# Kernel optimization log

Measured on AMD Instinct MI355X. Metric: run time of the kernel, lower is better.

The kernel has to match this reference:

```python
import jax, jax.numpy as jnp
import numpy as np

B, S, H = 32, 512, 768
N, E, P = 4096, 131072, 65536
HEADS1, C1 = 4, 128
HEADS2, C2 = 1, 64
NUM_REL, REL_HID = 6, 256
NER_HID, NER_LAB = 256, 9
LRELU_SLOPE = 0.2  # PyG GATConv default negative_slope
LN_EPS = 1e-5


def setup_inputs() -> dict:
    key = jax.random.key(0)
    ks = jax.random.split(key, 24)
    sc = 0.02
    inp = {
        'sequence_output': jax.random.normal(ks[0], (B, S, H), jnp.float32),
        'ent_start': jax.random.randint(ks[1], (N,), 0, S - 8),
        'ent_len': jax.random.randint(ks[2], (N,), 0, 8),
        'ent_batch': jax.random.randint(ks[3], (N,), 0, B),
        'edge_index': jax.random.randint(ks[4], (2, E), 0, N),
        'pair_idx': jax.random.randint(ks[5], (P, 2), 0, N),
        'W1': jax.random.normal(ks[6], (H, HEADS1 * C1), jnp.float32) * sc,
        'a_src1': jax.random.normal(ks[7], (HEADS1, C1), jnp.float32) * sc,
        'a_dst1': jax.random.normal(ks[8], (HEADS1, C1), jnp.float32) * sc,
        'b1': jnp.zeros((HEADS1 * C1,), jnp.float32),
        'W2': jax.random.normal(ks[9], (HEADS1 * C1, HEADS2 * C2), jnp.float32) * sc,
        'a_src2': jax.random.normal(ks[10], (HEADS2, C2), jnp.float32) * sc,
        'a_dst2': jax.random.normal(ks[11], (HEADS2, C2), jnp.float32) * sc,
        'b2': jnp.zeros((HEADS2 * C2,), jnp.float32),
        # 6 per-relation classifiers: Linear(128,256)+LN+ReLU+Linear(256,1)
        'relW1': jax.random.normal(ks[12], (NUM_REL, 2 * C2, REL_HID), jnp.float32) * sc,
        'relb1': jnp.zeros((NUM_REL, REL_HID), jnp.float32),
        'ln_g': jnp.ones((NUM_REL, REL_HID), jnp.float32),
        'ln_b': jnp.zeros((NUM_REL, REL_HID), jnp.float32),
        'relW2': jax.random.normal(ks[13], (NUM_REL, REL_HID, 1), jnp.float32) * sc,
        'relb2': jnp.zeros((NUM_REL, 1), jnp.float32),
        # NER head: Linear(768,256)+ReLU+Linear(256,9)
        'nerW1': jax.random.normal(ks[14], (H, NER_HID), jnp.float32) * sc,
        'nerb1': jnp.zeros((NER_HID,), jnp.float32),
        'nerW2': jax.random.normal(ks[15], (NER_HID, NER_LAB), jnp.float32) * sc,
        'nerb2': jnp.zeros((NER_LAB,), jnp.float32),
    }
    return inp


def _gat(x, src, dst, W, a_src, a_dst, b, heads, ch, n):
    # PyG GATConv: per-head linear, additive attention, softmax over incoming edges
    h = (x @ W).reshape(n, heads, ch)                      # [N,Hd,C]
    e_src = jnp.sum(h * a_src, axis=-1)                    # [N,Hd]
    e_dst = jnp.sum(h * a_dst, axis=-1)
    e = jax.nn.leaky_relu(e_src[src] + e_dst[dst], LRELU_SLOPE)  # [E,Hd]
    m = jax.ops.segment_max(e, dst, num_segments=n)
    ex = jnp.exp(e - m[dst])
    denom = jax.ops.segment_sum(ex, dst, num_segments=n)
    alpha = ex / denom[dst]                                # [E,Hd]
    out = jax.ops.segment_sum(alpha[:, :, None] * h[src], dst, num_segments=n)
    return out.reshape(n, heads * ch) + b


def reference(sequence_output, ent_start, ent_len, ent_batch, edge_index, pair_idx,
              W1, a_src1, a_dst1, b1, W2, a_src2, a_dst2, b2,
              relW1, relb1, ln_g, ln_b, relW2, relb2,
              nerW1, nerb1, nerW2, nerb2):
    n = ent_start.shape[0]
    # NER head on the full sequence
    ner_logits = jax.nn.relu(sequence_output @ nerW1 + nerb1) @ nerW2 + nerb2  # [B,S,9]
    # Entity-span mean pooling via exclusive prefix sums (inclusive span start..start+len)
    csum = jnp.cumsum(sequence_output, axis=1)
    csum = jnp.concatenate([jnp.zeros((B, 1, H), sequence_output.dtype), csum], axis=1)  # [B,S+1,H]
    ent_end = ent_start + ent_len
    span_sum = csum[ent_batch, ent_end + 1] - csum[ent_batch, ent_start]  # [N,H]
    x = span_sum / (ent_len + 1).astype(span_sum.dtype)[:, None]
    # add self loops (PyG GATConv default add_self_loops=True)
    loops = jnp.arange(n, dtype=edge_index.dtype)
    src = jnp.concatenate([edge_index[0], loops])
    dst = jnp.concatenate([edge_index[1], loops])
    x = _gat(x, src, dst, W1, a_src1, a_dst1, b1, HEADS1, C1, n)
    x = jax.nn.relu(x)  # dropout p=0.3 is identity in eval mode
    x = _gat(x, src, dst, W2, a_src2, a_dst2, b2, HEADS2, C2, n)  # [N,64]
    # Pair features: cat(x[e1], x[e2]) -> [P,128]
    pair_feat = jnp.concatenate([x[pair_idx[:, 0]], x[pair_idx[:, 1]]], axis=-1)
    # All 6 relation classifiers, vectorized over the relation dim
    hid = jnp.einsum('pf,rfk->rpk', pair_feat, relW1) + relb1[:, None, :]  # [6,P,256]
    mu = jnp.mean(hid, axis=-1, keepdims=True)
    var = jnp.mean(jnp.square(hid - mu), axis=-1, keepdims=True)
    hid = (hid - mu) * jax.lax.rsqrt(var + LN_EPS) * ln_g[:, None, :] + ln_b[:, None, :]
    hid = jax.nn.relu(hid)
    rel_logits = (jnp.einsum('rpk,rko->rpo', hid, relW2) + relb2[:, None, :])[..., 0]  # [6,P]
    return ner_logits, rel_logits
```

## Files before the change

### kernel.cpp

```cpp
#include <hip/hip_runtime.h>
#include <math.h>

#define LRELU 0.2f

constexpr int Bn = 32, Sn = 512, Hn = 768, Nn = 4096, En = 131072, Pn = 65536;
constexpr int ET = En + Nn;

typedef __attribute__((ext_vector_type(8))) short bf16x8;
typedef __attribute__((ext_vector_type(4))) float f32x4;

constexpr size_t OFF_X0  = 0;
constexpr size_t OFF_UV  = 0;
constexpr size_t OFF_H1  = 4194304;
constexpr size_t OFF_X1  = OFF_H1  + 2097152;
constexpr size_t OFF_H2  = OFF_X1  + 2097152;
constexpr size_t OFF_X2  = OFF_H2  + 262144;
constexpr size_t OFF_ES1 = OFF_X2  + 262144;
constexpr size_t OFF_ED1 = OFF_ES1 + 16384;
constexpr size_t OFF_ES2 = OFF_ED1 + 16384;
constexpr size_t OFF_ED2 = OFF_ES2 + 4096;
constexpr size_t OFF_ROW = OFF_ED2 + 4096;
constexpr size_t OFF_CUR = OFF_ROW + 4104;
constexpr size_t OFF_EDG = OFF_CUR + 4096;
constexpr size_t OFF_W1S = OFF_EDG + 135168;
constexpr size_t OFF_NW1S = OFF_W1S + 196608;
constexpr size_t OFF_W2S = OFF_NW1S + 98304;

__device__ __forceinline__ short f2bf(float f) {
  union { float f; unsigned u; } x; x.f = f;
  unsigned r = x.u + 0x7fff + ((x.u >> 16) & 1);
  return (short)(r >> 16);
}
__device__ __forceinline__ float bf2f(short s) {
  union { unsigned u; float f; } x;
  x.u = ((unsigned)(unsigned short)s) << 16;
  return x.f;
}

__global__ __launch_bounds__(256) void span_pool_k(
    const float* __restrict__ seq, const int* __restrict__ est,
    const int* __restrict__ eln, const int* __restrict__ ebt,
    float* __restrict__ x0) {
  int idx = blockIdx.x * 256 + threadIdx.x;
  if (idx >= Nn * (Hn / 4)) return;
  int e = idx / (Hn / 4);
  int c = (idx % (Hn / 4)) * 4;
  int s0 = est[e], L = eln[e] + 1, b = ebt[e];
  const float* p = seq + ((size_t)b * Sn + s0) * Hn + c;
  float ax = 0, ay = 0, az = 0, aw = 0;
  for (int i = 0; i < L; ++i) {
    float4 v = *(const float4*)(p + (size_t)i * Hn);
    ax += v.x; ay += v.y; az += v.z; aw += v.w;
  }
  float inv = 1.0f / (float)L;
  float4 o; o.x = ax * inv; o.y = ay * inv; o.z = az * inv; o.w = aw * inv;
  *(float4*)&x0[(size_t)e * Hn + c] = o;
}

template <int EPI, int NTW, int KC>
__global__ __launch_bounds__(256) void mfma_gemm_k(
    const float* __restrict__ A, const short* __restrict__ Bswz,
    float* __restrict__ C, const float* __restrict__ bias,
    int M, int K, int N) {
  constexpr int RS = KC + 8;
  __shared__ short at[64 * RS];
  int t = threadIdx.x;
  size_t rowb = (size_t)blockIdx.x * 64;
  int colb = blockIdx.y * (64 * NTW);
  int w = t >> 6, lane = t & 63, quad = lane >> 4, id = lane & 15;
  f32x4 acc[4][NTW];
#pragma unroll
  for (int mt = 0; mt < 4; ++mt)
#pragma unroll
    for (int nt = 0; nt < NTW; ++nt) acc[mt][nt] = (f32x4){0.f, 0.f, 0.f, 0.f};

  for (int k0 = 0; k0 < K; k0 += KC) {
    constexpr int CH = 64 * KC / 8 / 256;
#pragma unroll
    for (int i = 0; i < CH; ++i) {
      int cid = t + i * 256;
      int p = cid / (KC / 8), o8 = (cid % (KC / 8)) * 8;
      const float* src = &A[(rowb + p) * (size_t)K + k0 + o8];
      float4 v0 = *(const float4*)src;
      float4 v1 = *(const float4*)(src + 4);
      bf16x8 bv;
      bv[0] = f2bf(v0.x); bv[1] = f2bf(v0.y); bv[2] = f2bf(v0.z); bv[3] = f2bf(v0.w);
      bv[4] = f2bf(v1.x); bv[5] = f2bf(v1.y); bv[6] = f2bf(v1.z); bv[7] = f2bf(v1.w);
      *(bf16x8*)&at[p * RS + o8] = bv;
    }
    __syncthreads();
#pragma unroll
    for (int kk = 0; kk < KC / 32; ++kk) {
      bf16x8 af[4], bfr[NTW];
#pragma unroll
      for (int mt = 0; mt < 4; ++mt)
        af[mt] = *(const bf16x8*)&at[(mt * 16 + id) * RS + kk * 32 + quad * 8];
#pragma unroll
      for (int nt = 0; nt < NTW; ++nt) {
        int ntg = (colb >> 4) + w * NTW + nt;
        bfr[nt] = *(const bf16x8*)&Bswz[(((size_t)(k0 >> 5) + kk) * (N >> 4) + ntg) * 512 + lane * 8];
      }
#pragma unroll
      for (int mt = 0; mt < 4; ++mt)
#pragma unroll
        for (int nt = 0; nt < NTW; ++nt)
          acc[mt][nt] = __builtin_amdgcn_mfma_f32_16x16x32_bf16(af[mt], bfr[nt], acc[mt][nt], 0, 0, 0);
    }
    __syncthreads();
  }
#pragma unroll
  for (int nt = 0; nt < NTW; ++nt) {
    int col = colb + w * (16 * NTW) + nt * 16 + id;
#pragma unroll
    for (int mt = 0; mt < 4; ++mt) {
#pragma unroll
      for (int reg = 0; reg < 4; ++reg) {
        size_t row = rowb + mt * 16 + quad * 4 + reg;
        float v = acc[mt][nt][reg];
        if (EPI == 3) {
          int r = col >> 9, rem = col & 511;
          if (rem < 256) v += bias[(r << 8) + rem];
          ((short*)C)[((size_t)r * Nn + row) * 512 + rem] = f2bf(v);
        } else if (EPI == 2) {
          ((short*)C)[row * (size_t)N + col] = f2bf(v);
        } else {
          C[row * (size_t)N + col] = v;
        }
      }
    }
  }
}

template <int MT>
__global__ __launch_bounds__(256) void ner_fused_k(
    const float* __restrict__ A, const short* __restrict__ Bswz,
    const float* __restrict__ W2, const float* __restrict__ b1,
    const float* __restrict__ b2, float* __restrict__ out) {
  constexpr int K = 768;
  constexpr int RS = 136, HS = 264, WS = 260;
  constexpr int MW = MT / 16;
  __shared__ short at[MT * RS];
  __shared__ short hid[MT * HS];
  __shared__ float w2t[9 * WS];
  __shared__ float b2l[9];
  int t = threadIdx.x;
  size_t rowb = (size_t)blockIdx.x * MT;
  for (int u = t; u < 2304; u += 256) {
    int k = u / 9, jj = u % 9;
    w2t[jj * WS + k] = W2[u];
  }
  if (t < 9) b2l[t] = b2[t];
  int w = t >> 6, lane = t & 63, quad = lane >> 4, id = lane & 15;
  f32x4 acc[MW][4];
#pragma unroll
  for (int mt = 0; mt < MW; ++mt)
#pragma unroll
    for (int nt = 0; nt < 4; ++nt) acc[mt][nt] = (f32x4){0.f, 0.f, 0.f, 0.f};

  for (int k0 = 0; k0 < K; k0 += 128) {
#pragma unroll
    for (int i = 0; i < MT / 16; ++i) {
      int cid = t + i * 256;
      int p = cid >> 4, o8 = (cid & 15) * 8;
      const float* src = &A[(rowb + p) * (size_t)K + k0 + o8];
      float4 v0 = *(const float4*)src;
      float4 v1 = *(const float4*)(src + 4);
      bf16x8 bv;
      bv[0] = f2bf(v0.x); bv[1] = f2bf(v0.y); bv[2] = f2bf(v0.z); bv[3] = f2bf(v0.w);
      bv[4] = f2bf(v1.x); bv[5] = f2bf(v1.y); bv[6] = f2bf(v1.z); bv[7] = f2bf(v1.w);
      *(bf16x8*)&at[p * RS + o8] = bv;
    }
    __syncthreads();
#pragma unroll
    for (int kk = 0; kk < 4; ++kk) {
      bf16x8 af[MW], bfr[4];
#pragma unroll
      for (int mt = 0; mt < MW; ++mt)
        af[mt] = *(const bf16x8*)&at[(mt * 16 + id) * RS + kk * 32 + quad * 8];
#pragma unroll
      for (int nt = 0; nt < 4; ++nt) {
        int ntg = w * 4 + nt;
        bfr[nt] = *(const bf16x8*)&Bswz[(((size_t)(k0 >> 5) + kk) * 16 + ntg) * 512 + lane * 8];
      }
#pragma unroll
      for (int mt = 0; mt < MW; ++mt)
#pragma unroll
        for (int nt = 0; nt < 4; ++nt)
          acc[mt][nt] = __builtin_amdgcn_mfma_f32_16x16x32_bf16(af[mt], bfr[nt], acc[mt][nt], 0, 0, 0);
    }
    __syncthreads();
  }
#pragma unroll
  for (int nt = 0; nt < 4; ++nt) {
    int col = w * 64 + nt * 16 + id;
    float bb = b1[col];
#pragma unroll
    for (int mt = 0; mt < MW; ++mt)
#pragma unroll
      for (int reg = 0; reg < 4; ++reg) {
        int row = mt * 16 + quad * 4 + reg;
        hid[row * HS + col] = f2bf(fmaxf(acc[mt][nt][reg] + bb, 0.f));
      }
  }
  __syncthreads();
  for (int u = t; u < MT * 9; u += 256) {
    int row = u / 9, jj = u % 9;
    const short* hp = &hid[row * HS];
    const float* wp = &w2t[jj * WS];
    float a = 0.f;
#pragma unroll
    for (int k8 = 0; k8 < 256; k8 += 8) {
      bf16x8 hv = *(const bf16x8*)&hp[k8];
      float4 w0 = *(const float4*)&wp[k8];
      float4 w1 = *(const float4*)&wp[k8 + 4];
      a += bf2f(hv[0]) * w0.x + bf2f(hv[1]) * w0.y + bf2f(hv[2]) * w0.z + bf2f(hv[3]) * w0.w;
      a += bf2f(hv[4]) * w1.x + bf2f(hv[5]) * w1.y + bf2f(hv[6]) * w1.z + bf2f(hv[7]) * w1.w;
    }
    out[(rowb + row) * 9 + jj] = a + b2l[jj];
  }
}

__device__ __forceinline__ void swz_store(short* __restrict__ o, int k, int n, int N, float v) {
  int kk = k >> 5, quad = (k >> 3) & 3, j = k & 7, ntg = n >> 4, id = n & 15;
  o[(((size_t)kk * (N >> 4)) + ntg) * 512 + (quad * 16 + id) * 8 + j] = f2bf(v);
}

__global__ void swz_all_k(const float* __restrict__ W1, const float* __restrict__ nW1,
                          const float* __restrict__ W2, short* __restrict__ w1s,
                          short* __restrict__ nw1s, short* __restrict__ w2s) {
  int i = blockIdx.x * 256 + threadIdx.x;
  if (i < 768 * 512) {
    swz_store(w1s, i / 512, i % 512, 512, W1[i]);
  } else if (i < 768 * 512 + 768 * 256) {
    int i2 = i - 768 * 512;
    swz_store(nw1s, i2 / 256, i2 % 256, 256, nW1[i2]);
  } else if (i < 768 * 512 + 768 * 256 + 512 * 64) {
    int i2 = i - (768 * 512 + 768 * 256);
    swz_store(w2s, i2 / 64, i2 % 64, 64, W2[i2]);
  }
}

__global__ void swz_uv_k(const float* __restrict__ rW1, short* __restrict__ o) {
  int i = blockIdx.x * 256 + threadIdx.x;
  if (i >= 6 * 128 * 256) return;
  int n = i & 255, k = (i >> 8) & 127, r = i >> 15;
  int c = r * 512 + (k >> 6) * 256 + n;
  int kr = k & 63;
  int kk = kr >> 5, quad = (kr >> 3) & 3, j = kr & 7, ntg = c >> 4, id = c & 15;
  o[(((size_t)kk * 192) + ntg) * 512 + (quad * 16 + id) * 8 + j] = f2bf(rW1[i]);
}

template <int HD, int C>
__global__ __launch_bounds__(256) void coef_b_k(
    const short* __restrict__ h, const float* __restrict__ a_src,
    const float* __restrict__ a_dst, float* __restrict__ es, float* __restrict__ ed) {
  int idx = blockIdx.x * 256 + threadIdx.x;
  if (idx >= Nn * HD) return;
  int n = idx / HD, hd = idx % HD;
  const short* hp = h + (size_t)n * HD * C + hd * C;
  const float* sp = a_src + hd * C;
  const float* dp = a_dst + hd * C;
  float s = 0, d = 0;
  for (int c = 0; c < C; c += 8) {
    bf16x8 v = *(const bf16x8*)(hp + c);
#pragma unroll
    for (int k = 0; k < 8; ++k) {
      float f = bf2f(v[k]);
      s += f * sp[c + k];
      d += f * dp[c + k];
    }
  }
  es[idx] = s; ed[idx] = d;
}

__global__ void zero_k(int* __restrict__ p, int n) {
  int i = blockIdx.x * 256 + threadIdx.x;
  if (i < n) p[i] = 0;
}

__global__ void count_k(const int* __restrict__ eidx, int* __restrict__ cnt) {
  int i = blockIdx.x * 256 + threadIdx.x;
  if (i >= ET) return;
  int dst = (i < En) ? eidx[En + i] : (i - En);
  atomicAdd(&cnt[dst], 1);
}

__global__ __launch_bounds__(256) void scan_k(int* cnt_cur, int* rowoff) {
  __shared__ int s[256];
  int t = threadIdx.x;
  int loc[16]; int run = 0; int base = t * 16;
#pragma unroll
  for (int i = 0; i < 16; ++i) { loc[i] = run; run += cnt_cur[base + i]; }
  s[t] = run;
  __syncthreads();
  for (int off = 1; off < 256; off <<= 1) {
    int v = (t >= off) ? s[t - off] : 0;
    __syncthreads();
    s[t] += v;
    __syncthreads();
  }
  int offset = (t > 0) ? s[t - 1] : 0;
#pragma unroll
  for (int i = 0; i < 16; ++i) {
    int o = offset + loc[i];
    rowoff[base + i] = o;
    cnt_cur[base + i] = o;
  }
  if (t == 255) rowoff[4096] = s[255];
}

__global__ void scatter_k(const int* __restrict__ eidx, int* __restrict__ cur,
                          int* __restrict__ esrc) {
  int i = blockIdx.x * 256 + threadIdx.x;
  if (i >= ET) return;
  int s, d;
  if (i < En) { s = eidx[i]; d = eidx[En + i]; } else { s = d = i - En; }
  int pos = atomicAdd(&cur[d], 1);
  esrc[pos] = s;
}

template <int HD, int C, bool RELU>
__global__ __launch_bounds__(256) void gat_agg_k(
    const short* __restrict__ h, const float* __restrict__ es,
    const float* __restrict__ ed, const int* __restrict__ row_off,
    const int* __restrict__ eslist, const float* __restrict__ bias,
    float* __restrict__ xout) {
  constexpr int HDC = HD * C, OCT = HDC / 8, JS = 256 / OCT;
  constexpr int CAP = 320;
  __shared__ float red[256];
  __shared__ float mxs[HD], dns[HD];
  __shared__ float exc[CAP * HD];
  __shared__ float part[JS * HDC];
  int n = blockIdx.x, t = threadIdx.x;
  int ro = row_off[n], deg = row_off[n + 1] - ro;
  int hd = t % HD, ei = t / HD;
  constexpr int ES = 256 / HD;
  float edv = ed[n * HD + hd];
  float pm = -3.402823466e38f;
  for (int j = ei; j < deg; j += ES) {
    int s = eslist[ro + j];
    float e = es[s * HD + hd] + edv;
    e = (e > 0.f) ? e : LRELU * e;
    pm = fmaxf(pm, e);
  }
  red[t] = pm;
  __syncthreads();
  for (int off = 128; off >= HD; off >>= 1) {
    if (t < off) red[t] = fmaxf(red[t], red[t + off]);
    __syncthreads();
  }
  if (t < HD) mxs[t] = red[t];
  __syncthreads();
  float mx = mxs[hd];
  float ps = 0.f;
  for (int j = ei; j < deg; j += ES) {
    int s = eslist[ro + j];
    float e = es[s * HD + hd] + edv;
    e = (e > 0.f) ? e : LRELU * e;
    float ex = __expf(e - mx);
    if (j < CAP) exc[j * HD + hd] = ex;
    ps += ex;
  }
  red[t] = ps;
  __syncthreads();
  for (int off = 128; off >= HD; off >>= 1) {
    if (t < off) red[t] += red[t + off];
    __syncthreads();
  }
  if (t < HD) dns[t] = red[t];
  __syncthreads();
  int oc = t % OCT, js = t / OCT;
  int hh = oc / (C / 8);
  float mxh = mxs[hh], edh = ed[n * HD + hh];
  float a[8];
#pragma unroll
  for (int k = 0; k < 8; ++k) a[k] = 0.f;
  for (int j = js; j < deg; j += JS) {
    int s = eslist[ro + j];
    float ex;
    if (j < CAP) ex = exc[j * HD + hh];
    else {
      float e = es[s * HD + hh] + edh;
      e = (e > 0.f) ? e : LRELU * e;
      ex = __expf(e - mxh);
    }
    bf16x8 hv = *(const bf16x8*)&h[(size_t)s * HDC + oc * 8];
#pragma unroll
    for (int k = 0; k < 8; ++k) a[k] += ex * bf2f(hv[k]);
  }
#pragma unroll
  for (int k = 0; k < 8; ++k) part[js * HDC + oc * 8 + k] = a[k];
  __syncthreads();
  for (int c = t; c < HDC; c += 256) {
    float sum = 0.f;
#pragma unroll
    for (int q = 0; q < JS; ++q) sum += part[q * HDC + c];
    int hh2 = c / C;
    float v = sum / dns[hh2] + bias[c];
    if (RELU) v = fmaxf(v, 0.f);
    xout[(size_t)n * HDC + c] = v;
  }
}

__global__ __launch_bounds__(256) void pair_rel_k(
    const short* __restrict__ UV, const int* __restrict__ pidx,
    const float* __restrict__ lng, const float* __restrict__ lnb,
    const float* __restrict__ rW2, const float* __restrict__ rb2,
    float* __restrict__ out) {
  int t = threadIdx.x;
  int r = blockIdx.y;
  int w = t >> 6, lane = t & 63;
  int pg = lane >> 4, l16 = lane & 15;
  float g[16], bb[16], wv[16];
  int cb = r * 256 + l16 * 16;
#pragma unroll
  for (int q = 0; q < 4; ++q) {
    *(float4*)&g[q * 4]  = *(const float4*)&lng[cb + q * 4];
    *(float4*)&bb[q * 4] = *(const float4*)&lnb[cb + q * 4];
    *(float4*)&wv[q * 4] = *(const float4*)&rW2[cb + q * 4];
  }
  float rb2v = rb2[r];
  const short* UVr = UV + (size_t)r * Nn * 512;
  int pbase = blockIdx.x * 256 + w * 64;
  for (int it = 0; it < 16; ++it) {
    int p = pbase + it * 4 + pg;
    int i = pidx[p * 2], j = pidx[p * 2 + 1];
    const short* up = &UVr[(size_t)i * 512 + l16 * 16];
    const short* vp = &UVr[(size_t)j * 512 + 256 + l16 * 16];
    bf16x8 u0 = *(const bf16x8*)up, u1 = *(const bf16x8*)(up + 8);
    bf16x8 v0 = *(const bf16x8*)vp, v1 = *(const bf16x8*)(vp + 8);
    float hv[16], s1 = 0.f, s2 = 0.f;
#pragma unroll
    for (int cc = 0; cc < 8; ++cc) {
      float h = bf2f(u0[cc]) + bf2f(v0[cc]);
      hv[cc] = h; s1 += h; s2 += h * h;
    }
#pragma unroll
    for (int cc = 0; cc < 8; ++cc) {
      float h = bf2f(u1[cc]) + bf2f(v1[cc]);
      hv[8 + cc] = h; s1 += h; s2 += h * h;
    }
#pragma unroll
    for (int off = 1; off < 16; off <<= 1) {
      s1 += __shfl_xor(s1, off, 64);
      s2 += __shfl_xor(s2, off, 64);
    }
    float mu = s1 * (1.f / 256.f);
    float var = s2 * (1.f / 256.f) - mu * mu;
    float rs = rsqrtf(var + 1e-5f);
    float pv = 0.f;
#pragma unroll
    for (int cc = 0; cc < 16; ++cc) {
      float v = (hv[cc] - mu) * rs * g[cc] + bb[cc];
      v = fmaxf(v, 0.f);
      pv += v * wv[cc];
    }
#pragma unroll
    for (int off = 1; off < 16; off <<= 1) pv += __shfl_xor(pv, off, 64);
    if (l16 == 0) out[(size_t)r * Pn + p] = pv + rb2v;
  }
}

extern "C" void kernel_launch(void* const* d_in, const int* in_sizes, int n_in,
                              void* d_out, int out_size, void* d_ws, size_t ws_size,
                              hipStream_t stream) {
  const float* seq = (const float*)d_in[0];
  const int* est = (const int*)d_in[1];
  const int* eln = (const int*)d_in[2];
  const int* ebt = (const int*)d_in[3];
  const int* eidx = (const int*)d_in[4];
  const int* pidx = (const int*)d_in[5];
  const float* W1 = (const float*)d_in[6];
  const float* as1 = (const float*)d_in[7];
  const float* ad1 = (const float*)d_in[8];
  const float* b1 = (const float*)d_in[9];
  const float* W2 = (const float*)d_in[10];
  const float* as2 = (const float*)d_in[11];
  const float* ad2 = (const float*)d_in[12];
  const float* b2 = (const float*)d_in[13];
  const float* rW1 = (const float*)d_in[14];
  const float* rb1 = (const float*)d_in[15];
  const float* lng = (const float*)d_in[16];
  const float* lnb = (const float*)d_in[17];
  const float* rW2 = (const float*)d_in[18];
  const float* rb2 = (const float*)d_in[19];
  const float* nW1 = (const float*)d_in[20];
  const float* nb1 = (const float*)d_in[21];
  const float* nW2 = (const float*)d_in[22];
  const float* nb2 = (const float*)d_in[23];
  float* out = (float*)d_out;
  float* ws = (float*)d_ws;

  float* x0 = ws + OFF_X0;
  short* uv = (short*)(ws + OFF_UV);
  short* h1 = (short*)(ws + OFF_H1);
  float* x1 = ws + OFF_X1;
  short* h2 = (short*)(ws + OFF_H2);
  short* uvw = (short*)(ws + OFF_H2);
  float* x2 = ws + OFF_X2;
  float* es1 = ws + OFF_ES1;
  float* ed1 = ws + OFF_ED1;
  float* es2 = ws + OFF_ES2;
  float* ed2 = ws + OFF_ED2;
  int* rowoff = (int*)(ws + OFF_ROW);
  int* cur = (int*)(ws + OFF_CUR);
  int* edg = (int*)(ws + OFF_EDG);
  short* w1s = (short*)(ws + OFF_W1S);
  short* nw1s = (short*)(ws + OFF_NW1S);
  short* w2s = (short*)(ws + OFF_W2S);

  zero_k<<<16, 256, 0, stream>>>(cur, Nn);
  count_k<<<(ET + 255) / 256, 256, 0, stream>>>(eidx, cur);
  scan_k<<<1, 256, 0, stream>>>(cur, rowoff);
  scatter_k<<<(ET + 255) / 256, 256, 0, stream>>>(eidx, cur, edg);
  swz_all_k<<<(768 * 512 + 768 * 256 + 512 * 64 + 255) / 256, 256, 0, stream>>>(
      W1, nW1, W2, w1s, nw1s, w2s);

  span_pool_k<<<Nn * (Hn / 4) / 256, 256, 0, stream>>>(seq, est, eln, ebt, x0);

  mfma_gemm_k<2, 2, 128><<<dim3(Nn / 64, 512 / 128), 256, 0, stream>>>(x0, w1s, (float*)h1, nullptr, Nn, Hn, 512);
  coef_b_k<4, 128><<<(Nn * 4) / 256, 256, 0, stream>>>(h1, as1, ad1, es1, ed1);
  gat_agg_k<4, 128, true><<<Nn, 256, 0, stream>>>(h1, es1, ed1, rowoff, edg, b1, x1);

  mfma_gemm_k<2, 1, 128><<<dim3(Nn / 64, 1), 256, 0, stream>>>(x1, w2s, (float*)h2, nullptr, Nn, 512, 64);
  coef_b_k<1, 64><<<(Nn + 255) / 256, 256, 0, stream>>>(h2, as2, ad2, es2, ed2);
  gat_agg_k<1, 64, false><<<Nn, 256, 0, stream>>>(h2, es2, ed2, rowoff, edg, b2, x2);

  swz_uv_k<<<(6 * 128 * 256) / 256, 256, 0, stream>>>(rW1, uvw);
  mfma_gemm_k<3, 2, 64><<<dim3(Nn / 64, 3072 / 128), 256, 0, stream>>>(x2, uvw, (float*)uv, rb1, Nn, 64, 3072);
  pair_rel_k<<<dim3(Pn / 256, 6), 256, 0, stream>>>(uv, pidx, lng, lnb, rW2, rb2,
                                                    out + (size_t)Bn * Sn * 9);

  ner_fused_k<32><<<(Bn * Sn) / 32, 256, 0, stream>>>(seq, nw1s, nW2, nb1, nb2, out);
}
```

Measured before the change: 347.6 us.

## Sort relation pairs by first entity and enlarge NER row tile

Builds a counting-sort bucket list of pairs keyed by the first entity index, using count, scan and atomic-scatter kernels. The pair classifier then reads (i, j, p) from that list, so consecutive pairs share U rows for better cache locality, and writes each result back to its original index. Separately, the fused NER kernel's row tile grows from 32 to 64, so each block reuses its loaded weights across twice as many rows, at the cost of more registers and shared memory. The sort adds four small launches and reuses the x1 workspace region, which is only safe if x1 is no longer read after the second GEMM.

```diff
diff --git a/kernel.cpp b/kernel.cpp
--- a/kernel.cpp
+++ b/kernel.cpp
@@ -131,35 +131,33 @@
   }
 }
 
-template <int MT>
 __global__ __launch_bounds__(256) void ner_fused_k(
     const float* __restrict__ A, const short* __restrict__ Bswz,
     const float* __restrict__ W2, const float* __restrict__ b1,
     const float* __restrict__ b2, float* __restrict__ out) {
   constexpr int K = 768;
   constexpr int RS = 136, HS = 264, WS = 260;
-  constexpr int MW = MT / 16;
-  __shared__ short at[MT * RS];
-  __shared__ short hid[MT * HS];
+  __shared__ short at[64 * RS];
+  __shared__ short hid[64 * HS];
   __shared__ float w2t[9 * WS];
   __shared__ float b2l[9];
   int t = threadIdx.x;
-  size_t rowb = (size_t)blockIdx.x * MT;
+  size_t rowb = (size_t)blockIdx.x * 64;
   for (int u = t; u < 2304; u += 256) {
     int k = u / 9, jj = u % 9;
     w2t[jj * WS + k] = W2[u];
   }
   if (t < 9) b2l[t] = b2[t];
   int w = t >> 6, lane = t & 63, quad = lane >> 4, id = lane & 15;
-  f32x4 acc[MW][4];
-#pragma unroll
-  for (int mt = 0; mt < MW; ++mt)
+  f32x4 acc[4][4];
+#pragma unroll
+  for (int mt = 0; mt < 4; ++mt)
 #pragma unroll
     for (int nt = 0; nt < 4; ++nt) acc[mt][nt] = (f32x4){0.f, 0.f, 0.f, 0.f};
 
   for (int k0 = 0; k0 < K; k0 += 128) {
 #pragma unroll
-    for (int i = 0; i < MT / 16; ++i) {
+    for (int i = 0; i < 4; ++i) {
       int cid = t + i * 256;
       int p = cid >> 4, o8 = (cid & 15) * 8;
       const float* src = &A[(rowb + p) * (size_t)K + k0 + o8];
@@ -173,9 +171,9 @@
     __syncthreads();
 #pragma unroll
     for (int kk = 0; kk < 4; ++kk) {
-      bf16x8 af[MW], bfr[4];
-#pragma unroll
-      for (int mt = 0; mt < MW; ++mt)
+      bf16x8 af[4], bfr[4];
+#pragma unroll
+      for (int mt = 0; mt < 4; ++mt)
         af[mt] = *(const bf16x8*)&at[(mt * 16 + id) * RS + kk * 32 + quad * 8];
 #pragma unroll
       for (int nt = 0; nt < 4; ++nt) {
@@ -183,7 +181,7 @@
         bfr[nt] = *(const bf16x8*)&Bswz[(((size_t)(k0 >> 5) + kk) * 16 + ntg) * 512 + lane * 8];
       }
 #pragma unroll
-      for (int mt = 0; mt < MW; ++mt)
+      for (int mt = 0; mt < 4; ++mt)
 #pragma unroll
         for (int nt = 0; nt < 4; ++nt)
           acc[mt][nt] = __builtin_amdgcn_mfma_f32_16x16x32_bf16(af[mt], bfr[nt], acc[mt][nt], 0, 0, 0);
@@ -195,7 +193,7 @@
     int col = w * 64 + nt * 16 + id;
     float bb = b1[col];
 #pragma unroll
-    for (int mt = 0; mt < MW; ++mt)
+    for (int mt = 0; mt < 4; ++mt)
 #pragma unroll
       for (int reg = 0; reg < 4; ++reg) {
         int row = mt * 16 + quad * 4 + reg;
@@ -203,7 +201,7 @@
       }
   }
   __syncthreads();
-  for (int u = t; u < MT * 9; u += 256) {
+  for (int u = t; u < 576; u += 256) {
     int row = u / 9, jj = u % 9;
     const short* hp = &hid[row * HS];
     const float* wp = &w2t[jj * WS];
@@ -317,6 +315,20 @@
   if (i < En) { s = eidx[i]; d = eidx[En + i]; } else { s = d = i - En; }
   int pos = atomicAdd(&cur[d], 1);
   esrc[pos] = s;
+}
+
+__global__ void pcount_k(const int* __restrict__ pidx, int* __restrict__ cnt) {
+  int p = blockIdx.x * 256 + threadIdx.x;
+  if (p < Pn) atomicAdd(&cnt[pidx[2 * p]], 1);
+}
+
+__global__ void pscatter3_k(const int* __restrict__ pidx, int* __restrict__ cur,
+                            int4* __restrict__ plist) {
+  int p = blockIdx.x * 256 + threadIdx.x;
+  if (p >= Pn) return;
+  int i = pidx[2 * p], j = pidx[2 * p + 1];
+  int pos = atomicAdd(&cur[i], 1);
+  plist[pos] = make_int4(i, j, p, 0);
 }
 
 template <int HD, int C, bool RELU>
@@ -403,7 +415,7 @@
 }
 
 __global__ __launch_bounds__(256) void pair_rel_k(
-    const short* __restrict__ UV, const int* __restrict__ pidx,
+    const short* __restrict__ UV, const int4* __restrict__ plist,
     const float* __restrict__ lng, const float* __restrict__ lnb,
     const float* __restrict__ rW2, const float* __restrict__ rb2,
     float* __restrict__ out) {
@@ -421,12 +433,11 @@
   }
   float rb2v = rb2[r];
   const short* UVr = UV + (size_t)r * Nn * 512;
-  int pbase = blockIdx.x * 256 + w * 64;
+  int qbase = blockIdx.x * 256 + w * 64;
   for (int it = 0; it < 16; ++it) {
-    int p = pbase + it * 4 + pg;
-    int i = pidx[p * 2], j = pidx[p * 2 + 1];
-    const short* up = &UVr[(size_t)i * 512 + l16 * 16];
-    const short* vp = &UVr[(size_t)j * 512 + 256 + l16 * 16];
+    int4 ijp = plist[qbase + it * 4 + pg];
+    const short* up = &UVr[(size_t)ijp.x * 512 + l16 * 16];
+    const short* vp = &UVr[(size_t)ijp.y * 512 + 256 + l16 * 16];
     bf16x8 u0 = *(const bf16x8*)up, u1 = *(const bf16x8*)(up + 8);
     bf16x8 v0 = *(const bf16x8*)vp, v1 = *(const bf16x8*)(vp + 8);
     float hv[16], s1 = 0.f, s2 = 0.f;
@@ -457,7 +468,7 @@
     }
 #pragma unroll
     for (int off = 1; off < 16; off <<= 1) pv += __shfl_xor(pv, off, 64);
-    if (l16 == 0) out[(size_t)r * Pn + p] = pv + rb2v;
+    if (l16 == 0) out[(size_t)r * Pn + ijp.z] = pv + rb2v;
   }
 }
 
@@ -508,6 +519,9 @@
   short* w1s = (short*)(ws + OFF_W1S);
   short* nw1s = (short*)(ws + OFF_NW1S);
   short* w2s = (short*)(ws + OFF_W2S);
+  int* prow = (int*)(ws + OFF_X1);
+  int* pcur = (int*)(ws + OFF_X1 + 4104);
+  int4* plist = (int4*)(ws + OFF_X1 + 8208);
 
   zero_k<<<16, 256, 0, stream>>>(cur, Nn);
   count_k<<<(ET + 255) / 256, 256, 0, stream>>>(eidx, cur);
@@ -523,13 +537,19 @@
   gat_agg_k<4, 128, true><<<Nn, 256, 0, stream>>>(h1, es1, ed1, rowoff, edg, b1, x1);
 
   mfma_gemm_k<2, 1, 128><<<dim3(Nn / 64, 1), 256, 0, stream>>>(x1, w2s, (float*)h2, nullptr, Nn, 512, 64);
+
+  zero_k<<<16, 256, 0, stream>>>(pcur, Nn);
+  pcount_k<<<Pn / 256, 256, 0, stream>>>(pidx, pcur);
+  scan_k<<<1, 256, 0, stream>>>(pcur, prow);
+  pscatter3_k<<<Pn / 256, 256, 0, stream>>>(pidx, pcur, plist);
+
   coef_b_k<1, 64><<<(Nn + 255) / 256, 256, 0, stream>>>(h2, as2, ad2, es2, ed2);
   gat_agg_k<1, 64, false><<<Nn, 256, 0, stream>>>(h2, es2, ed2, rowoff, edg, b2, x2);
 
   swz_uv_k<<<(6 * 128 * 256) / 256, 256, 0, stream>>>(rW1, uvw);
   mfma_gemm_k<3, 2, 64><<<dim3(Nn / 64, 3072 / 128), 256, 0, stream>>>(x2, uvw, (float*)uv, rb1, Nn, 64, 3072);
-  pair_rel_k<<<dim3(Pn / 256, 6), 256, 0, stream>>>(uv, pidx, lng, lnb, rW2, rb2,
+  pair_rel_k<<<dim3(Pn / 256, 6), 256, 0, stream>>>(uv, plist, lng, lnb, rW2, rb2,
                                                     out + (size_t)Bn * Sn * 9);
 
-  ner_fused_k<32><<<(Bn * Sn) / 32, 256, 0, stream>>>(seq, nw1s, nW2, nb1, nb2, out);
-}
+  ner_fused_k<<<(Bn * Sn) / 64, 256, 0, stream>>>(seq, nw1s, nW2, nb1, nb2, out);
+}
```

New measurement: 369.0 us. 6.2% more time.
